# Kernel tuning notes

Measured on AMD Instinct MI355X. Metric: run time of the kernel, lower is better.

Reference implementation:

```python
import jax, jax.numpy as jnp
import numpy as np

N = 200_000   # nodes
E = 3_200_000 # edges (avg degree 16)
M = 100_000   # scored indices
NE = 32       # num_examples
C = 32        # CHANNELS
H = 1024      # HIDDEN_LAYER
NT = 11       # NODE_TYPES
L = 8         # RESIDUAL_LAYERS
EPS = 1e-5


def setup_inputs() -> dict:
    key = jax.random.key(0)
    ks = jax.random.split(key, 16)
    xn = lambda k, shape, s=1.0: s * jax.random.normal(k, shape, dtype=jnp.float32)
    std = float(np.sqrt(2.0 / (C + C // 2)))  # xavier_normal_ for (C, C//2)
    return {
        "num_examples": NE,
        "assignment": jnp.sort(jax.random.randint(ks[0], (N,), 0, NE, dtype=jnp.int32)),
        "nodes": jax.random.randint(ks[1], (N,), 0, NT, dtype=jnp.int32),
        "src": jax.random.randint(ks[2], (E,), 0, N, dtype=jnp.int32),
        "dst": jax.random.randint(ks[3], (E,), 0, N, dtype=jnp.int32),
        "indices": jnp.sort(jax.random.randint(ks[4], (M,), 0, N, dtype=jnp.int32)),
        "emb": xn(ks[5], (NT, C)),
        "w0_out": xn(ks[6], (C, C // 2), std),
        "w0_back": xn(ks[7], (C, C // 2), std),
        "bn1_gamma": jnp.ones((L, C), jnp.float32),
        "bn1_beta": jnp.zeros((L, C), jnp.float32),
        "w1_out": xn(ks[8], (L, C, C // 2), std),
        "w1_back": xn(ks[9], (L, C, C // 2), std),
        "bn2_gamma": jnp.ones((L, C), jnp.float32),
        "bn2_beta": jnp.zeros((L, C), jnp.float32),
        "w2_out": xn(ks[10], (L, C, C // 2), std),
        "w2_back": xn(ks[11], (L, C, C // 2), std),
        "wh": xn(ks[12], (C, H), 0.05),
        "bh": jnp.zeros((H,), jnp.float32),
        "wo": xn(ks[13], (H, 1), 0.05),
        "bo": jnp.zeros((1,), jnp.float32),
    }


def reference(num_examples, assignment, nodes, src, dst, indices, emb,
              w0_out, w0_back, bn1_gamma, bn1_beta, w1_out, w1_back,
              bn2_gamma, bn2_beta, w2_out, w2_back, wh, bh, wo, bo):
    n = nodes.shape[0]

    def agg(x, s, d):  # sparse A @ x with A[d, s] = 1
        return jax.ops.segment_sum(x[s], d, num_segments=n)

    def biconv(x, w_o, w_b):
        out = agg(x @ w_o, src, dst)    # adjacency @ x @ W_out
        back = agg(x @ w_b, dst, src)   # adjacency_t @ x @ W_back
        return jnp.concatenate([out, back], axis=1)  # [n, C]

    def bn(x, g, b):  # BatchNorm1d, batch statistics (biased var)
        m = jnp.mean(x, axis=0)
        v = jnp.var(x, axis=0)
        return (x - m) * jax.lax.rsqrt(v + EPS) * g + b

    x = emb[nodes]                      # [n, C]
    x = biconv(x, w0_out, w0_back)

    def step(x, p):
        g1, b1, o1, k1, g2, b2, o2, k2 = p
        h = jax.nn.relu(bn(x, g1, b1))
        h = biconv(h, o1, k1)
        h = jax.nn.relu(bn(h, g2, b2))
        h = biconv(h, o2, k2)
        return x + h, None

    x, _ = jax.lax.scan(step, x, (bn1_gamma, bn1_beta, w1_out, w1_back,
                                  bn2_gamma, bn2_beta, w2_out, w2_back))

    sel = x[indices]                                        # [M, C]
    s = jax.nn.relu(jax.nn.relu(sel) @ wh + bh) @ wo + bo   # [M, 1]
    s = s[:, 0]
    seg = assignment[indices]                               # per-example group ids (sorted)
    mx = jax.lax.stop_gradient(jax.ops.segment_max(s, seg, num_segments=num_examples))
    sh = s - mx[seg]
    lse = jnp.log(jax.ops.segment_sum(jnp.exp(sh), seg, num_segments=num_examples))
    return sh - lse[seg]                                    # log_softmax per example, concatenated
```

## Files before the change

### kernel.cpp

```cpp
#include <hip/hip_runtime.h>
#include <math.h>

#define N_NODES 200000
#define N_EDGES 3200000
#define M_SEL   100000
#define NEX     32
#define NT      11
#define CH      32
#define HID     1024
#define NL      8
#define BN_EPS  1e-5f

#define BSHIFT  9
#define BSIZE   512
#define KB      391
#define PAYMASK 0x3FFFF

__device__ __forceinline__ unsigned bf16_bits(float f) {
  unsigned u = __float_as_uint(f);
  return (u + 0x7fffu + ((u >> 16) & 1u)) >> 16;
}
__device__ __forceinline__ unsigned pack_bf2(float lo, float hi) {
  return bf16_bits(lo) | (bf16_bits(hi) << 16);
}
#define BF_LO(u) __uint_as_float((u) << 16)
#define BF_HI(u) __uint_as_float((u) & 0xffff0000u)

__global__ void __launch_bounds__(256) bin_count_kernel(
    const int* __restrict__ src, const int* __restrict__ dst,
    int* __restrict__ bcnt_in, int* __restrict__ bcnt_out) {
  __shared__ int h_in[KB], h_out[KB];
  int tid = threadIdx.x;
  for (int i = tid; i < KB; i += 256) { h_in[i] = 0; h_out[i] = 0; }
  __syncthreads();
  for (int e = blockIdx.x * 256 + tid; e < N_EDGES; e += gridDim.x * 256) {
    atomicAdd(&h_in[dst[e] >> BSHIFT], 1);
    atomicAdd(&h_out[src[e] >> BSHIFT], 1);
  }
  __syncthreads();
  for (int b = tid; b < KB; b += 256) {
    if (h_in[b])  atomicAdd(&bcnt_in[b], h_in[b]);
    if (h_out[b]) atomicAdd(&bcnt_out[b], h_out[b]);
  }
}

__global__ void __launch_bounds__(256) bucket_scan_kernel(
    const int* __restrict__ bcnt_in, int* __restrict__ boff_in, int* __restrict__ gcur_in,
    const int* __restrict__ bcnt_out, int* __restrict__ boff_out, int* __restrict__ gcur_out) {
  __shared__ int s[512];
  __shared__ int wtot[4];
  int tid = threadIdx.x;
  int lane = tid & 63, wid = tid >> 6;
  for (int dir = 0; dir < 2; dir++) {
    const int* bcnt = dir ? bcnt_out : bcnt_in;
    int* boff = dir ? boff_out : boff_in;
    int* gcur = dir ? gcur_out : gcur_in;
    int i0 = 2 * tid, i1 = 2 * tid + 1;
    int a0 = (i0 < KB) ? bcnt[i0] : 0;
    int a1 = (i1 < KB) ? bcnt[i1] : 0;
    int pair = a0 + a1;
    int incl = pair;
#pragma unroll
    for (int o = 1; o < 64; o <<= 1) { int t = __shfl_up(incl, o); if (lane >= o) incl += t; }
    if (lane == 63) wtot[wid] = incl;
    __syncthreads();
    if (tid == 0) { int r = 0; for (int w = 0; w < 4; w++) { int v = wtot[w]; wtot[w] = r; r += v; } }
    __syncthreads();
    int exclp = incl - pair + wtot[wid];
    s[i0] = exclp;
    s[i1] = exclp + a0;
    __syncthreads();
    for (int b = tid; b < KB; b += 256) { boff[b] = s[b]; gcur[b] = s[b]; }
    if (i0 == KB - 1) boff[KB] = s[i0] + a0;
    if (i1 == KB - 1) boff[KB] = s[i1] + a1;
    __syncthreads();
  }
}

__global__ void __launch_bounds__(256) stage_kernel(
    const int* __restrict__ src, const int* __restrict__ dst,
    int* __restrict__ gcur_in, unsigned* __restrict__ staging_in,
    int* __restrict__ gcur_out, unsigned* __restrict__ staging_out) {
  __shared__ int cnt[KB], cur[KB];
  int tid = threadIdx.x;
  int dir = blockIdx.y;
  const int* key = dir ? src : dst;
  const int* pay = dir ? dst : src;
  int* gcur = dir ? gcur_out : gcur_in;
  unsigned* staging = dir ? staging_out : staging_in;
  for (int i = tid; i < KB; i += 256) cnt[i] = 0;
  __syncthreads();
  int e0 = blockIdx.x * 4096;
#pragma unroll
  for (int j = 0; j < 16; j++) {
    int e = e0 + j * 256 + tid;
    if (e < N_EDGES) atomicAdd(&cnt[key[e] >> BSHIFT], 1);
  }
  __syncthreads();
  for (int b = tid; b < KB; b += 256) {
    int c = cnt[b];
    cur[b] = c ? atomicAdd(&gcur[b], c) : 0;
  }
  __syncthreads();
#pragma unroll
  for (int j = 0; j < 16; j++) {
    int e = e0 + j * 256 + tid;
    if (e < N_EDGES) {
      int k = key[e];
      int b = k >> BSHIFT;
      int p = atomicAdd(&cur[b], 1);
      staging[p] = ((unsigned)(k & (BSIZE - 1)) << 18) | (unsigned)pay[e];
    }
  }
}

__global__ void __launch_bounds__(256) build_kernel(
    const unsigned* __restrict__ staging_in, const int* __restrict__ boff_in,
    int* __restrict__ off_in, int* __restrict__ csr_in,
    const unsigned* __restrict__ staging_out, const int* __restrict__ boff_out,
    int* __restrict__ off_out, int* __restrict__ csr_out) {
  __shared__ int cnt[BSIZE];
  __shared__ int wtot[4];
  int tid = threadIdx.x;
  int b = blockIdx.x;
  int dir = blockIdx.y;
  const unsigned* staging = dir ? staging_out : staging_in;
  const int* boff = dir ? boff_out : boff_in;
  int* off = dir ? off_out : off_in;
  int* csr = dir ? csr_out : csr_in;
  int ebase = boff[b], eend = boff[b + 1];
  int node_base = b << BSHIFT;
  int nnodes = min(BSIZE, N_NODES - node_base);
  cnt[2 * tid] = 0; cnt[2 * tid + 1] = 0;
  __syncthreads();
  for (int e = ebase + tid; e < eend; e += 256)
    atomicAdd(&cnt[staging[e] >> 18], 1);
  __syncthreads();
  int i0 = 2 * tid, i1 = 2 * tid + 1;
  int a0 = cnt[i0], a1 = cnt[i1];
  int pair = a0 + a1;
  int lane = tid & 63, wid = tid >> 6;
  int incl = pair;
#pragma unroll
  for (int o = 1; o < 64; o <<= 1) { int t = __shfl_up(incl, o); if (lane >= o) incl += t; }
  if (lane == 63) wtot[wid] = incl;
  __syncthreads();
  if (tid == 0) { int r = 0; for (int w = 0; w < 4; w++) { int v = wtot[w]; wtot[w] = r; r += v; } }
  __syncthreads();
  int exclp = incl - pair + wtot[wid];
  cnt[i0] = exclp;
  cnt[i1] = exclp + a0;
  __syncthreads();
  for (int i = tid; i < nnodes; i += 256) off[node_base + i] = ebase + cnt[i];
  if (b == KB - 1 && tid == 0) off[N_NODES] = boff[KB];
  __syncthreads();
  for (int e = ebase + tid; e < eend; e += 256) {
    unsigned rec = staging[e];
    int p = atomicAdd(&cnt[rec >> 18], 1);
    csr[ebase + p] = (int)(rec & PAYMASK);
  }
}

__device__ __forceinline__ void store_split(unsigned short* y_out,
                                            unsigned short* y_back,
                                            int i, const float* acc) {
  uint4 t0, t1;
  t0.x = pack_bf2(acc[0], acc[1]);   t0.y = pack_bf2(acc[2], acc[3]);
  t0.z = pack_bf2(acc[4], acc[5]);   t0.w = pack_bf2(acc[6], acc[7]);
  t1.x = pack_bf2(acc[8], acc[9]);   t1.y = pack_bf2(acc[10], acc[11]);
  t1.z = pack_bf2(acc[12], acc[13]); t1.w = pack_bf2(acc[14], acc[15]);
  uint4* po = (uint4*)(y_out + (size_t)i * 16);
  po[0] = t0; po[1] = t1;
  t0.x = pack_bf2(acc[16], acc[17]); t0.y = pack_bf2(acc[18], acc[19]);
  t0.z = pack_bf2(acc[20], acc[21]); t0.w = pack_bf2(acc[22], acc[23]);
  t1.x = pack_bf2(acc[24], acc[25]); t1.y = pack_bf2(acc[26], acc[27]);
  t1.z = pack_bf2(acc[28], acc[29]); t1.w = pack_bf2(acc[30], acc[31]);
  uint4* pb = (uint4*)(y_back + (size_t)i * 16);
  pb[0] = t0; pb[1] = t1;
}

__global__ void __launch_bounds__(256) emb_mm_kernel(
    const int* __restrict__ nodes, const float* __restrict__ emb,
    const float* __restrict__ w_out, const float* __restrict__ w_back,
    unsigned short* __restrict__ y_out, unsigned short* __restrict__ y_back) {
  __shared__ float W[CH][CH];
  __shared__ float Esh[NT * CH];
  int tid = threadIdx.x;
  for (int t = tid; t < CH * CH; t += blockDim.x) {
    int k = t >> 5, j = t & 31;
    W[k][j] = (j < 16) ? w_out[k * 16 + j] : w_back[k * 16 + j - 16];
  }
  for (int t = tid; t < NT * CH; t += blockDim.x) Esh[t] = emb[t];
  __syncthreads();
  int i = blockIdx.x * blockDim.x + tid;
  if (i >= N_NODES) return;
  int tn = nodes[i];
  float v[CH];
#pragma unroll
  for (int k = 0; k < CH; k++) v[k] = Esh[tn * CH + k];
  float acc[CH];
#pragma unroll
  for (int j = 0; j < CH; j++) acc[j] = 0.f;
#pragma unroll
  for (int k = 0; k < CH; k++) {
    float vk = v[k];
#pragma unroll
    for (int j = 0; j < CH; j++) acc[j] += vk * W[k][j];
  }
  store_split(y_out, y_back, i, acc);
}

__global__ void __launch_bounds__(256) bn_relu_mm_kernel(
    const float* __restrict__ xin, const float* __restrict__ stats,
    const float* __restrict__ gamma, const float* __restrict__ beta,
    const float* __restrict__ w_out, const float* __restrict__ w_back,
    unsigned short* __restrict__ y_out, unsigned short* __restrict__ y_back) {
  __shared__ float W[CH][CH];
  __shared__ float sc[CH], sh[CH];
  int tid = threadIdx.x;
  for (int t = tid; t < CH * CH; t += blockDim.x) {
    int k = t >> 5, j = t & 31;
    W[k][j] = (j < 16) ? w_out[k * 16 + j] : w_back[k * 16 + j - 16];
  }
  if (tid < CH) {
    float m  = stats[tid] * (1.0f / N_NODES);
    float s2 = stats[CH + tid] * (1.0f / N_NODES);
    float var = s2 - m * m;
    float scale = gamma[tid] * rsqrtf(var + BN_EPS);
    sc[tid] = scale;
    sh[tid] = beta[tid] - m * scale;
  }
  __syncthreads();
  int i = blockIdx.x * blockDim.x + tid;
  if (i >= N_NODES) return;
  const float4* xp = (const float4*)(xin + (size_t)i * CH);
  float v[CH];
#pragma unroll
  for (int q = 0; q < 8; q++) {
    float4 t = xp[q];
    v[4 * q + 0] = fmaxf(t.x * sc[4 * q + 0] + sh[4 * q + 0], 0.f);
    v[4 * q + 1] = fmaxf(t.y * sc[4 * q + 1] + sh[4 * q + 1], 0.f);
    v[4 * q + 2] = fmaxf(t.z * sc[4 * q + 2] + sh[4 * q + 2], 0.f);
    v[4 * q + 3] = fmaxf(t.w * sc[4 * q + 3] + sh[4 * q + 3], 0.f);
  }
  float acc[CH];
#pragma unroll
  for (int j = 0; j < CH; j++) acc[j] = 0.f;
#pragma unroll
  for (int k = 0; k < CH; k++) {
    float vk = v[k];
#pragma unroll
    for (int j = 0; j < CH; j++) acc[j] += vk * W[k][j];
  }
  store_split(y_out, y_back, i, acc);
}

__global__ void __launch_bounds__(256) agg_dir_kernel(
    const unsigned short* __restrict__ y_out, const unsigned short* __restrict__ y_back,
    const float* __restrict__ xres, float* __restrict__ out,
    const int* __restrict__ off_in, const int* __restrict__ csr_in,
    const int* __restrict__ off_out, const int* __restrict__ csr_out,
    float* __restrict__ stats) {
  __shared__ float ssum[CH], sssq[CH];
  int tid = threadIdx.x;
  if (tid < CH) { ssum[tid] = 0.f; sssq[tid] = 0.f; }
  __syncthreads();
  int dir = blockIdx.y;
  const unsigned short* y = dir ? y_back : y_out;
  const int* off = dir ? off_out : off_in;
  const int* csr = dir ? csr_out : csr_in;
  int chanbase = dir * 16;
  int t = blockIdx.x * 256 + tid;
  bool valid = t < 2 * N_NODES;
  int q = t & 1;
  int i = valid ? (t >> 1) : 0;
  int lo = 0, hi = 0;
  if (valid) { lo = off[i]; hi = off[i + 1]; }
  int q8 = q * 8;
  float a0 = 0.f, a1 = 0.f, a2 = 0.f, a3 = 0.f;
  float a4 = 0.f, a5 = 0.f, a6 = 0.f, a7 = 0.f;
  int e = lo;
  for (; e + 8 <= hi; e += 8) {
    int n0 = csr[e + 0], n1 = csr[e + 1], n2 = csr[e + 2], n3 = csr[e + 3];
    int n4 = csr[e + 4], n5 = csr[e + 5], n6 = csr[e + 6], n7 = csr[e + 7];
    uint4 p0 = *(const uint4*)(y + (size_t)n0 * 16 + q8);
    uint4 p1 = *(const uint4*)(y + (size_t)n1 * 16 + q8);
    uint4 p2 = *(const uint4*)(y + (size_t)n2 * 16 + q8);
    uint4 p3 = *(const uint4*)(y + (size_t)n3 * 16 + q8);
    uint4 p4 = *(const uint4*)(y + (size_t)n4 * 16 + q8);
    uint4 p5 = *(const uint4*)(y + (size_t)n5 * 16 + q8);
    uint4 p6 = *(const uint4*)(y + (size_t)n6 * 16 + q8);
    uint4 p7 = *(const uint4*)(y + (size_t)n7 * 16 + q8);
    a0 += BF_LO(p0.x) + BF_LO(p1.x) + BF_LO(p2.x) + BF_LO(p3.x)
        + BF_LO(p4.x) + BF_LO(p5.x) + BF_LO(p6.x) + BF_LO(p7.x);
    a1 += BF_HI(p0.x) + BF_HI(p1.x) + BF_HI(p2.x) + BF_HI(p3.x)
        + BF_HI(p4.x) + BF_HI(p5.x) + BF_HI(p6.x) + BF_HI(p7.x);
    a2 += BF_LO(p0.y) + BF_LO(p1.y) + BF_LO(p2.y) + BF_LO(p3.y)
        + BF_LO(p4.y) + BF_LO(p5.y) + BF_LO(p6.y) + BF_LO(p7.y);
    a3 += BF_HI(p0.y) + BF_HI(p1.y) + BF_HI(p2.y) + BF_HI(p3.y)
        + BF_HI(p4.y) + BF_HI(p5.y) + BF_HI(p6.y) + BF_HI(p7.y);
    a4 += BF_LO(p0.z) + BF_LO(p1.z) + BF_LO(p2.z) + BF_LO(p3.z)
        + BF_LO(p4.z) + BF_LO(p5.z) + BF_LO(p6.z) + BF_LO(p7.z);
    a5 += BF_HI(p0.z) + BF_HI(p1.z) + BF_HI(p2.z) + BF_HI(p3.z)
        + BF_HI(p4.z) + BF_HI(p5.z) + BF_HI(p6.z) + BF_HI(p7.z);
    a6 += BF_LO(p0.w) + BF_LO(p1.w) + BF_LO(p2.w) + BF_LO(p3.w)
        + BF_LO(p4.w) + BF_LO(p5.w) + BF_LO(p6.w) + BF_LO(p7.w);
    a7 += BF_HI(p0.w) + BF_HI(p1.w) + BF_HI(p2.w) + BF_HI(p3.w)
        + BF_HI(p4.w) + BF_HI(p5.w) + BF_HI(p6.w) + BF_HI(p7.w);
  }
  for (; e + 4 <= hi; e += 4) {
    int n0 = csr[e + 0], n1 = csr[e + 1], n2 = csr[e + 2], n3 = csr[e + 3];
    uint4 p0 = *(const uint4*)(y + (size_t)n0 * 16 + q8);
    uint4 p1 = *(const uint4*)(y + (size_t)n1 * 16 + q8);
    uint4 p2 = *(const uint4*)(y + (size_t)n2 * 16 + q8);
    uint4 p3 = *(const uint4*)(y + (size_t)n3 * 16 + q8);
    a0 += BF_LO(p0.x) + BF_LO(p1.x) + BF_LO(p2.x) + BF_LO(p3.x);
    a1 += BF_HI(p0.x) + BF_HI(p1.x) + BF_HI(p2.x) + BF_HI(p3.x);
    a2 += BF_LO(p0.y) + BF_LO(p1.y) + BF_LO(p2.y) + BF_LO(p3.y);
    a3 += BF_HI(p0.y) + BF_HI(p1.y) + BF_HI(p2.y) + BF_HI(p3.y);
    a4 += BF_LO(p0.z) + BF_LO(p1.z) + BF_LO(p2.z) + BF_LO(p3.z);
    a5 += BF_HI(p0.z) + BF_HI(p1.z) + BF_HI(p2.z) + BF_HI(p3.z);
    a6 += BF_LO(p0.w) + BF_LO(p1.w) + BF_LO(p2.w) + BF_LO(p3.w);
    a7 += BF_HI(p0.w) + BF_HI(p1.w) + BF_HI(p2.w) + BF_HI(p3.w);
  }
  for (; e < hi; e++) {
    int nb = csr[e];
    uint4 p = *(const uint4*)(y + (size_t)nb * 16 + q8);
    a0 += BF_LO(p.x); a1 += BF_HI(p.x);
    a2 += BF_LO(p.y); a3 += BF_HI(p.y);
    a4 += BF_LO(p.z); a5 += BF_HI(p.z);
    a6 += BF_LO(p.w); a7 += BF_HI(p.w);
  }
  if (valid && xres) {
    const float4* rp = (const float4*)(xres + (size_t)i * CH + chanbase + q8);
    float4 r0 = rp[0], r1 = rp[1];
    a0 += r0.x; a1 += r0.y; a2 += r0.z; a3 += r0.w;
    a4 += r1.x; a5 += r1.y; a6 += r1.z; a7 += r1.w;
  }
  if (valid) {
    float4* op = (float4*)(out + (size_t)i * CH + chanbase + q8);
    op[0] = make_float4(a0, a1, a2, a3);
    op[1] = make_float4(a4, a5, a6, a7);
  }
  if (stats) {
    float s0 = a0 * a0, s1 = a1 * a1, s2 = a2 * a2, s3 = a3 * a3;
    float s4 = a4 * a4, s5 = a5 * a5, s6 = a6 * a6, s7 = a7 * a7;
#pragma unroll
    for (int o = 32; o >= 2; o >>= 1) {
      a0 += __shfl_down(a0, o); a1 += __shfl_down(a1, o);
      a2 += __shfl_down(a2, o); a3 += __shfl_down(a3, o);
      a4 += __shfl_down(a4, o); a5 += __shfl_down(a5, o);
      a6 += __shfl_down(a6, o); a7 += __shfl_down(a7, o);
      s0 += __shfl_down(s0, o); s1 += __shfl_down(s1, o);
      s2 += __shfl_down(s2, o); s3 += __shfl_down(s3, o);
      s4 += __shfl_down(s4, o); s5 += __shfl_down(s5, o);
      s6 += __shfl_down(s6, o); s7 += __shfl_down(s7, o);
    }
    if ((tid & 63) < 2) {
      int cb = chanbase + q8;
      atomicAdd(&ssum[cb + 0], a0); atomicAdd(&ssum[cb + 1], a1);
      atomicAdd(&ssum[cb + 2], a2); atomicAdd(&ssum[cb + 3], a3);
      atomicAdd(&ssum[cb + 4], a4); atomicAdd(&ssum[cb + 5], a5);
      atomicAdd(&ssum[cb + 6], a6); atomicAdd(&ssum[cb + 7], a7);
      atomicAdd(&sssq[cb + 0], s0); atomicAdd(&sssq[cb + 1], s1);
      atomicAdd(&sssq[cb + 2], s2); atomicAdd(&sssq[cb + 3], s3);
      atomicAdd(&sssq[cb + 4], s4); atomicAdd(&sssq[cb + 5], s5);
      atomicAdd(&sssq[cb + 6], s6); atomicAdd(&sssq[cb + 7], s7);
    }
    __syncthreads();
    if (tid < 16) {
      int c = chanbase + tid;
      atomicAdd(&stats[c], ssum[c]);
      atomicAdd(&stats[CH + c], sssq[c]);
    }
  }
}

__global__ void __launch_bounds__(256) score_kernel(
    const float* __restrict__ x, const int* __restrict__ indices,
    const int* __restrict__ assignment,
    const float* __restrict__ wh, const float* __restrict__ bh,
    const float* __restrict__ wo,
    float* __restrict__ s, int* __restrict__ seg) {
  __shared__ __align__(16) float s_wh[256][36];
  __shared__ float s_wo[256];
  __shared__ float s_bh[256];
  int tid = threadIdx.x;
  int mb = blockIdx.x >> 2;
  int tile = blockIdx.x & 3;
  int t0 = tile * 256;
  int m = mb * 256 + tid;
  bool valid = m < M_SEL;
  for (int u = tid; u < CH * 256; u += 256) {
    int k = u >> 8, jj = u & 255;
    s_wh[jj][k] = wh[(size_t)k * HID + t0 + jj];
  }
  s_wo[tid] = wo[t0 + tid];
  s_bh[tid] = bh[t0 + tid];
  __syncthreads();
  if (!valid) return;
  int idx = indices[m];
  float a[CH];
  const float4* xp = (const float4*)(x + (size_t)idx * CH);
#pragma unroll
  for (int q = 0; q < 8; q++) {
    float4 t = xp[q];
    a[4 * q + 0] = fmaxf(t.x, 0.f); a[4 * q + 1] = fmaxf(t.y, 0.f);
    a[4 * q + 2] = fmaxf(t.z, 0.f); a[4 * q + 3] = fmaxf(t.w, 0.f);
  }
  float sacc = 0.f;
  for (int jj = 0; jj < 256; jj++) {
    float h = s_bh[jj];
    const float4* wp = (const float4*)&s_wh[jj][0];
#pragma unroll
    for (int q = 0; q < 8; q++) {
      float4 w = wp[q];
      h += a[4 * q] * w.x + a[4 * q + 1] * w.y + a[4 * q + 2] * w.z + a[4 * q + 3] * w.w;
    }
    sacc += fmaxf(h, 0.f) * s_wo[jj];
  }
  atomicAdd(&s[m], sacc);
  if (tile == 0) seg[m] = assignment[idx];
}

__device__ __forceinline__ int lower_bound_dev(const int* a, int n, int key) {
  int lo = 0, hi = n;
  while (lo < hi) { int mid = (lo + hi) >> 1; if (a[mid] < key) lo = mid + 1; else hi = mid; }
  return lo;
}

__global__ void __launch_bounds__(256) logsoftmax_kernel(
    const float* __restrict__ s, const int* __restrict__ seg, float* __restrict__ out) {
  __shared__ float red[256];
  __shared__ int bounds[2];
  int tid = threadIdx.x;
  int b = blockIdx.x;
  if (tid == 0) {
    bounds[0] = lower_bound_dev(seg, M_SEL, b);
    bounds[1] = lower_bound_dev(seg, M_SEL, b + 1);
  }
  __syncthreads();
  int lo = bounds[0], hi = bounds[1];
  float mx = -INFINITY;
  for (int i = lo + tid; i < hi; i += 256) mx = fmaxf(mx, s[i]);
  red[tid] = mx; __syncthreads();
  for (int o = 128; o > 0; o >>= 1) { if (tid < o) red[tid] = fmaxf(red[tid], red[tid + o]); __syncthreads(); }
  float mxv = red[0];
  __syncthreads();
  float sum = 0.f;
  for (int i = lo + tid; i < hi; i += 256) sum += expf(s[i] - mxv);
  red[tid] = sum; __syncthreads();
  for (int o = 128; o > 0; o >>= 1) { if (tid < o) red[tid] += red[tid + o]; __syncthreads(); }
  float lse = logf(red[0]);
  for (int i = lo + tid; i < hi; i += 256) out[i] = (s[i] - mxv) - lse;
}

extern "C" void kernel_launch(void* const* d_in, const int* in_sizes, int n_in,
                              void* d_out, int out_size, void* d_ws, size_t ws_size,
                              hipStream_t stream) {
  const int*   assignment = (const int*)d_in[1];
  const int*   nodes      = (const int*)d_in[2];
  const int*   src        = (const int*)d_in[3];
  const int*   dst        = (const int*)d_in[4];
  const int*   indices    = (const int*)d_in[5];
  const float* emb        = (const float*)d_in[6];
  const float* w0_out     = (const float*)d_in[7];
  const float* w0_back    = (const float*)d_in[8];
  const float* bn1_gamma  = (const float*)d_in[9];
  const float* bn1_beta   = (const float*)d_in[10];
  const float* w1_out     = (const float*)d_in[11];
  const float* w1_back    = (const float*)d_in[12];
  const float* bn2_gamma  = (const float*)d_in[13];
  const float* bn2_beta   = (const float*)d_in[14];
  const float* w2_out     = (const float*)d_in[15];
  const float* w2_back    = (const float*)d_in[16];
  const float* wh         = (const float*)d_in[17];
  const float* bh         = (const float*)d_in[18];
  const float* wo         = (const float*)d_in[19];
  float* out = (float*)d_out;

  char* ws = (char*)d_ws;
  size_t off = 0;
  auto alloc = [&](size_t bytes) {
    char* p = ws + off;
    off = (off + bytes + 255) & ~(size_t)255;
    return p;
  };
  int* bcnt_in  = (int*)alloc((size_t)2 * KB * 4); int* bcnt_out = bcnt_in + KB;
  int* boff_in  = (int*)alloc((size_t)(KB + 1) * 4);
  int* boff_out = (int*)alloc((size_t)(KB + 1) * 4);
  int* gcur_in  = (int*)alloc((size_t)KB * 4);
  int* gcur_out = (int*)alloc((size_t)KB * 4);
  int* off_in   = (int*)alloc((size_t)(N_NODES + 1) * 4);
  int* off_out  = (int*)alloc((size_t)(N_NODES + 1) * 4);
  float* stats  = (float*)alloc((size_t)16 * 64 * 4);
  int* csr_in   = (int*)alloc((size_t)N_EDGES * 4);
  int* csr_out  = (int*)alloc((size_t)N_EDGES * 4);
  unsigned short* y_out  = (unsigned short*)alloc((size_t)N_NODES * 16 * 2);
  unsigned short* y_back = (unsigned short*)alloc((size_t)N_NODES * 16 * 2);
  float* xb = (float*)alloc((size_t)N_NODES * CH * 4);
  float* hb = (float*)alloc((size_t)N_NODES * CH * 4);
  float* sb = (float*)alloc((size_t)M_SEL * 4);
  int* segb = (int*)alloc((size_t)M_SEL * 4);
  unsigned* staging_in  = (unsigned*)xb;
  unsigned* staging_out = (unsigned*)xb + N_EDGES;

  hipMemsetAsync(bcnt_in, 0, (size_t)2 * KB * 4, stream);
  hipMemsetAsync(stats, 0, (size_t)16 * 64 * 4, stream);
  hipMemsetAsync(sb, 0, (size_t)M_SEL * 4, stream);

  bin_count_kernel<<<1024, 256, 0, stream>>>(src, dst, bcnt_in, bcnt_out);
  bucket_scan_kernel<<<1, 256, 0, stream>>>(bcnt_in, boff_in, gcur_in,
                                            bcnt_out, boff_out, gcur_out);
  dim3 gStage((N_EDGES + 4095) / 4096, 2);
  stage_kernel<<<gStage, 256, 0, stream>>>(src, dst, gcur_in, staging_in,
                                           gcur_out, staging_out);
  dim3 gBuild(KB, 2);
  build_kernel<<<gBuild, 256, 0, stream>>>(staging_in, boff_in, off_in, csr_in,
                                           staging_out, boff_out, off_out, csr_out);

  const int gA = (N_NODES + 255) / 256;
  dim3 gAgg((2 * N_NODES + 255) / 256, 2);
  auto agg_pass = [&](const float* xres, float* outb, float* st) {
    agg_dir_kernel<<<gAgg, 256, 0, stream>>>(y_out, y_back, xres, outb,
                                             off_in, csr_in, off_out, csr_out, st);
  };

  emb_mm_kernel<<<gA, 256, 0, stream>>>(nodes, emb, w0_out, w0_back, y_out, y_back);
  agg_pass(nullptr, xb, stats + 0 * 64);
  for (int l = 0; l < NL; l++) {
    bn_relu_mm_kernel<<<gA, 256, 0, stream>>>(xb, stats + (2 * l) * 64,
                                              bn1_gamma + l * CH, bn1_beta + l * CH,
                                              w1_out + l * CH * 16, w1_back + l * CH * 16,
                                              y_out, y_back);
    agg_pass(nullptr, hb, stats + (2 * l + 1) * 64);
    bn_relu_mm_kernel<<<gA, 256, 0, stream>>>(hb, stats + (2 * l + 1) * 64,
                                              bn2_gamma + l * CH, bn2_beta + l * CH,
                                              w2_out + l * CH * 16, w2_back + l * CH * 16,
                                              y_out, y_back);
    agg_pass(xb, xb, (l < NL - 1) ? (stats + (2 * l + 2) * 64) : nullptr);
  }
  score_kernel<<<4 * ((M_SEL + 255) / 256), 256, 0, stream>>>(
      xb, indices, assignment, wh, bh, wo, sb, segb);
  logsoftmax_kernel<<<NEX, 256, 0, stream>>>(sb, segb, out);
}
```

Measured before the change: 2.403 ms.

## Sort nodes by degree within 128-node windows to balance aggregation wavefronts

Adds a per-window bitonic sort kernel that orders the nodes in each 128-node window by degree and writes a permutation. The aggregation kernel reads this permutation, so threads in the same wavefront get neighbour lists of similar length and waste less time on divergent loop trip counts. The cost is one extra sort kernel per direction and an extra indirection load per thread. Writes to the output now follow the permuted node order, which may hurt store coalescing.

```diff
diff --git a/kernel.cpp b/kernel.cpp
--- a/kernel.cpp
+++ b/kernel.cpp
@@ -15,6 +15,7 @@
 #define BSIZE   512
 #define KB      391
 #define PAYMASK 0x3FFFF
+#define NWIN    1563
 
 __device__ __forceinline__ unsigned bf16_bits(float f) {
   unsigned u = __float_as_uint(f);
@@ -159,6 +160,38 @@
     int p = atomicAdd(&cnt[rec >> 18], 1);
     csr[ebase + p] = (int)(rec & PAYMASK);
   }
+}
+
+__global__ void __launch_bounds__(128) wsort_kernel(
+    const int* __restrict__ off_in, int* __restrict__ perm_in,
+    const int* __restrict__ off_out, int* __restrict__ perm_out) {
+  __shared__ int keys[128];
+  int t = threadIdx.x;
+  int dir = blockIdx.y;
+  const int* off = dir ? off_out : off_in;
+  int* perm = dir ? perm_out : perm_in;
+  int node = blockIdx.x * 128 + t;
+  int key = 0x7FFFFFFF;
+  if (node < N_NODES) {
+    int d = off[node + 1] - off[node];
+    if (d > 8191) d = 8191;
+    key = (d << 18) | node;
+  }
+  keys[t] = key;
+  __syncthreads();
+  for (int k = 2; k <= 128; k <<= 1) {
+    for (int j = k >> 1; j > 0; j >>= 1) {
+      int ixj = t ^ j;
+      if (ixj > t) {
+        int a = keys[t], b = keys[ixj];
+        bool asc = ((t & k) == 0);
+        if ((a > b) == asc) { keys[t] = b; keys[ixj] = a; }
+      }
+      __syncthreads();
+    }
+  }
+  int kk = keys[t];
+  perm[blockIdx.x * 128 + t] = (kk == 0x7FFFFFFF) ? -1 : (kk & PAYMASK);
 }
 
 __device__ __forceinline__ void store_split(unsigned short* y_out,
@@ -260,6 +293,7 @@
     const float* __restrict__ xres, float* __restrict__ out,
     const int* __restrict__ off_in, const int* __restrict__ csr_in,
     const int* __restrict__ off_out, const int* __restrict__ csr_out,
+    const int* __restrict__ perm_in, const int* __restrict__ perm_out,
     float* __restrict__ stats) {
   __shared__ float ssum[CH], sssq[CH];
   int tid = threadIdx.x;
@@ -269,11 +303,12 @@
   const unsigned short* y = dir ? y_back : y_out;
   const int* off = dir ? off_out : off_in;
   const int* csr = dir ? csr_out : csr_in;
+  const int* perm = dir ? perm_out : perm_in;
   int chanbase = dir * 16;
-  int t = blockIdx.x * 256 + tid;
-  bool valid = t < 2 * N_NODES;
-  int q = t & 1;
-  int i = valid ? (t >> 1) : 0;
+  int slot = blockIdx.x * 128 + (tid >> 1);
+  int i = perm[slot];
+  bool valid = i >= 0;
+  int q = tid & 1;
   int lo = 0, hi = 0;
   if (valid) { lo = off[i]; hi = off[i + 1]; }
   int q8 = q * 8;
@@ -496,6 +531,8 @@
   float* stats  = (float*)alloc((size_t)16 * 64 * 4);
   int* csr_in   = (int*)alloc((size_t)N_EDGES * 4);
   int* csr_out  = (int*)alloc((size_t)N_EDGES * 4);
+  int* perm_in  = (int*)alloc((size_t)NWIN * 128 * 4);
+  int* perm_out = (int*)alloc((size_t)NWIN * 128 * 4);
   unsigned short* y_out  = (unsigned short*)alloc((size_t)N_NODES * 16 * 2);
   unsigned short* y_back = (unsigned short*)alloc((size_t)N_NODES * 16 * 2);
   float* xb = (float*)alloc((size_t)N_NODES * CH * 4);
@@ -518,12 +555,15 @@
   dim3 gBuild(KB, 2);
   build_kernel<<<gBuild, 256, 0, stream>>>(staging_in, boff_in, off_in, csr_in,
                                            staging_out, boff_out, off_out, csr_out);
+  dim3 gSort(NWIN, 2);
+  wsort_kernel<<<gSort, 128, 0, stream>>>(off_in, perm_in, off_out, perm_out);
 
   const int gA = (N_NODES + 255) / 256;
-  dim3 gAgg((2 * N_NODES + 255) / 256, 2);
+  dim3 gAgg(NWIN, 2);
   auto agg_pass = [&](const float* xres, float* outb, float* st) {
     agg_dir_kernel<<<gAgg, 256, 0, stream>>>(y_out, y_back, xres, outb,
-                                             off_in, csr_in, off_out, csr_out, st);
+                                             off_in, csr_in, off_out, csr_out,
+                                             perm_in, perm_out, st);
   };
 
   emb_mm_kernel<<<gA, 256, 0, stream>>>(nodes, emb, w0_out, w0_back, y_out, y_back);
```

Result: no change. 2.406 ms (+0.1%).

## Compute score MLP hidden layer with bf16 MFMA instead of scalar FMA

Applied to the files above, without the earlier changes.

Replaces the scalar fp32 score kernel, which split the 1024 hidden units over four blocks and combined them with atomics, with an MFMA kernel. Each wave multiplies 16 selected rows by all of wh using 16x16x32 bf16 MFMA and fuses bias, ReLU and the wo dot product into a shuffle reduction. A small prep kernel repacks wh into bf16 fragment layout, and the memset of s plus its atomics are removed. This cuts the hidden-layer FLOP cost but rounds activations and weights to bf16 in the score path.

```diff
diff --git a/kernel.cpp b/kernel.cpp
--- a/kernel.cpp
+++ b/kernel.cpp
@@ -15,6 +15,9 @@
 #define BSIZE   512
 #define KB      391
 #define PAYMASK 0x3FFFF
+
+typedef __attribute__((ext_vector_type(8))) short bf16x8;
+typedef __attribute__((ext_vector_type(4))) float f32x4;
 
 __device__ __forceinline__ unsigned bf16_bits(float f) {
   unsigned u = __float_as_uint(f);
@@ -159,6 +162,19 @@
     int p = atomicAdd(&cnt[rec >> 18], 1);
     csr[ebase + p] = (int)(rec & PAYMASK);
   }
+}
+
+__global__ void __launch_bounds__(256) prep_whfrag_kernel(
+    const float* __restrict__ wh, unsigned short* __restrict__ wh_frag) {
+  int id = blockIdx.x * 256 + threadIdx.x;
+  if (id >= 64 * 64 * 8) return;
+  int t = id >> 9;
+  int rem = id & 511;
+  int lane = rem >> 3;
+  int i = rem & 7;
+  int k = (lane >> 4) * 8 + i;
+  int n = t * 16 + (lane & 15);
+  wh_frag[id] = (unsigned short)bf16_bits(wh[(size_t)k * HID + n]);
 }
 
 __device__ __forceinline__ void store_split(unsigned short* y_out,
@@ -376,51 +392,74 @@
   }
 }
 
-__global__ void __launch_bounds__(256) score_kernel(
+__global__ void __launch_bounds__(256) score_mfma_kernel(
     const float* __restrict__ x, const int* __restrict__ indices,
     const int* __restrict__ assignment,
-    const float* __restrict__ wh, const float* __restrict__ bh,
+    const unsigned short* __restrict__ wh_frag, const float* __restrict__ bh,
     const float* __restrict__ wo,
     float* __restrict__ s, int* __restrict__ seg) {
-  __shared__ __align__(16) float s_wh[256][36];
-  __shared__ float s_wo[256];
-  __shared__ float s_bh[256];
-  int tid = threadIdx.x;
-  int mb = blockIdx.x >> 2;
-  int tile = blockIdx.x & 3;
-  int t0 = tile * 256;
-  int m = mb * 256 + tid;
-  bool valid = m < M_SEL;
-  for (int u = tid; u < CH * 256; u += 256) {
-    int k = u >> 8, jj = u & 255;
-    s_wh[jj][k] = wh[(size_t)k * HID + t0 + jj];
-  }
-  s_wo[tid] = wo[t0 + tid];
-  s_bh[tid] = bh[t0 + tid];
-  __syncthreads();
-  if (!valid) return;
-  int idx = indices[m];
-  float a[CH];
-  const float4* xp = (const float4*)(x + (size_t)idx * CH);
-#pragma unroll
-  for (int q = 0; q < 8; q++) {
-    float4 t = xp[q];
-    a[4 * q + 0] = fmaxf(t.x, 0.f); a[4 * q + 1] = fmaxf(t.y, 0.f);
-    a[4 * q + 2] = fmaxf(t.z, 0.f); a[4 * q + 3] = fmaxf(t.w, 0.f);
-  }
-  float sacc = 0.f;
-  for (int jj = 0; jj < 256; jj++) {
-    float h = s_bh[jj];
-    const float4* wp = (const float4*)&s_wh[jj][0];
-#pragma unroll
-    for (int q = 0; q < 8; q++) {
-      float4 w = wp[q];
-      h += a[4 * q] * w.x + a[4 * q + 1] * w.y + a[4 * q + 2] * w.z + a[4 * q + 3] * w.w;
+  __shared__ __align__(16) unsigned short a_lds[64 * 32];
+  __shared__ float bh_lds[HID];
+  __shared__ float wo_lds[HID];
+  int tid = threadIdx.x;
+  int m0 = blockIdx.x * 64;
+#pragma unroll
+  for (int u = 0; u < 4; u++) {
+    bh_lds[u * 256 + tid] = bh[u * 256 + tid];
+    wo_lds[u * 256 + tid] = wo[u * 256 + tid];
+  }
+  {
+    int r = tid >> 2, part = tid & 3;
+    int m = m0 + r;
+    unsigned short* dstp = &a_lds[r * 32 + part * 8];
+    if (m < M_SEL) {
+      int idx = indices[m];
+      const float4* xp = (const float4*)(x + (size_t)idx * CH + part * 8);
+      float4 v0 = xp[0], v1 = xp[1];
+      uint4 packed;
+      packed.x = pack_bf2(fmaxf(v0.x, 0.f), fmaxf(v0.y, 0.f));
+      packed.y = pack_bf2(fmaxf(v0.z, 0.f), fmaxf(v0.w, 0.f));
+      packed.z = pack_bf2(fmaxf(v1.x, 0.f), fmaxf(v1.y, 0.f));
+      packed.w = pack_bf2(fmaxf(v1.z, 0.f), fmaxf(v1.w, 0.f));
+      *(uint4*)dstp = packed;
+      if (part == 0) seg[m] = assignment[idx];
+    } else {
+      *(uint4*)dstp = make_uint4(0, 0, 0, 0);
     }
-    sacc += fmaxf(h, 0.f) * s_wo[jj];
-  }
-  atomicAdd(&s[m], sacc);
-  if (tile == 0) seg[m] = assignment[idx];
+  }
+  __syncthreads();
+  int w = tid >> 6;
+  int lane = tid & 63;
+  int quad = lane >> 4;
+  int col = lane & 15;
+  bf16x8 afrag = *(const bf16x8*)&a_lds[(w * 16 + col) * 32 + quad * 8];
+  float racc0 = 0.f, racc1 = 0.f, racc2 = 0.f, racc3 = 0.f;
+  for (int t = 0; t < 64; t++) {
+    bf16x8 bfrag = *(const bf16x8*)&wh_frag[(size_t)(t * 64 + lane) * 8];
+    f32x4 c = __builtin_amdgcn_mfma_f32_16x16x32_bf16(afrag, bfrag,
+                                                      (f32x4){0.f, 0.f, 0.f, 0.f},
+                                                      0, 0, 0);
+    int n = t * 16 + col;
+    float bhv = bh_lds[n], wov = wo_lds[n];
+    racc0 += fmaxf(c[0] + bhv, 0.f) * wov;
+    racc1 += fmaxf(c[1] + bhv, 0.f) * wov;
+    racc2 += fmaxf(c[2] + bhv, 0.f) * wov;
+    racc3 += fmaxf(c[3] + bhv, 0.f) * wov;
+  }
+#pragma unroll
+  for (int o = 8; o >= 1; o >>= 1) {
+    racc0 += __shfl_xor(racc0, o);
+    racc1 += __shfl_xor(racc1, o);
+    racc2 += __shfl_xor(racc2, o);
+    racc3 += __shfl_xor(racc3, o);
+  }
+  if (col == 0) {
+    int mrow = m0 + w * 16 + quad * 4;
+    if (mrow + 0 < M_SEL) s[mrow + 0] = racc0;
+    if (mrow + 1 < M_SEL) s[mrow + 1] = racc1;
+    if (mrow + 2 < M_SEL) s[mrow + 2] = racc2;
+    if (mrow + 3 < M_SEL) s[mrow + 3] = racc3;
+  }
 }
 
 __device__ __forceinline__ int lower_bound_dev(const int* a, int n, int key) {
@@ -496,6 +535,7 @@
   float* stats  = (float*)alloc((size_t)16 * 64 * 4);
   int* csr_in   = (int*)alloc((size_t)N_EDGES * 4);
   int* csr_out  = (int*)alloc((size_t)N_EDGES * 4);
+  unsigned short* wh_frag = (unsigned short*)alloc((size_t)64 * 64 * 8 * 2);
   unsigned short* y_out  = (unsigned short*)alloc((size_t)N_NODES * 16 * 2);
   unsigned short* y_back = (unsigned short*)alloc((size_t)N_NODES * 16 * 2);
   float* xb = (float*)alloc((size_t)N_NODES * CH * 4);
@@ -507,7 +547,6 @@
 
   hipMemsetAsync(bcnt_in, 0, (size_t)2 * KB * 4, stream);
   hipMemsetAsync(stats, 0, (size_t)16 * 64 * 4, stream);
-  hipMemsetAsync(sb, 0, (size_t)M_SEL * 4, stream);
 
   bin_count_kernel<<<1024, 256, 0, stream>>>(src, dst, bcnt_in, bcnt_out);
   bucket_scan_kernel<<<1, 256, 0, stream>>>(bcnt_in, boff_in, gcur_in,
@@ -518,6 +557,7 @@
   dim3 gBuild(KB, 2);
   build_kernel<<<gBuild, 256, 0, stream>>>(staging_in, boff_in, off_in, csr_in,
                                            staging_out, boff_out, off_out, csr_out);
+  prep_whfrag_kernel<<<(64 * 64 * 8 + 255) / 256, 256, 0, stream>>>(wh, wh_frag);
 
   const int gA = (N_NODES + 255) / 256;
   dim3 gAgg((2 * N_NODES + 255) / 256, 2);
@@ -540,7 +580,7 @@
                                               y_out, y_back);
     agg_pass(xb, xb, (l < NL - 1) ? (stats + (2 * l + 2) * 64) : nullptr);
   }
-  score_kernel<<<4 * ((M_SEL + 255) / 256), 256, 0, stream>>>(
-      xb, indices, assignment, wh, bh, wo, sb, segb);
+  score_mfma_kernel<<<(M_SEL + 63) / 64, 256, 0, stream>>>(
+      xb, indices, assignment, wh_frag, bh, wo, sb, segb);
   logsoftmax_kernel<<<NEX, 256, 0, stream>>>(sb, segb, out);
 }
```

New measurement: 2.251 ms. 1.07x faster.
